# Kernel tuning notes

Hardware: AMD Instinct MI355X
Metric: run time of the kernel (lower is better)

## Reference

```python
import jax, jax.numpy as jnp
import numpy as np

DIMS = 1024; HEAD = 16; HD = DIMS // HEAD
MAX_DIST = 1024; MAX_SPAN = 1024; TEMP_SCALE = 0.01
SCALE = HD ** -0.25  # hd^-0.25 per the torch modules


def _layer_norm(x, g, b, eps=1e-5):
    m = jnp.mean(x, -1, keepdims=True)
    v = jnp.mean((x - m) ** 2, -1, keepdims=True)
    return (x - m) * jax.lax.rsqrt(v + eps) * g + b


def _forward(x, ln_a_g, ln_a_b, ln_b_g, ln_b_b, Wq, bq, Wk, Wv, bv, Wc, bc, Wp, bp, Wo, bo):
    B, S, D = x.shape
    local = _layer_norm(x, ln_a_g, ln_a_b)
    globe = _layer_norm(x, ln_b_g, ln_b_b)
    # --- global path: QueryModule/KeyModule/ValueModule + AttentionCombiner SDPA (mask=None) ---
    q = (globe @ Wq.T + bq).reshape(B, S, HEAD, HD).transpose(0, 2, 1, 3) * SCALE
    k = (globe @ Wk.T).reshape(B, S, HEAD, HD).transpose(0, 2, 1, 3) * SCALE
    v = (globe @ Wv.T + bv).reshape(B, S, HEAD, HD).transpose(0, 2, 1, 3)
    # SDPA applies its own 1/sqrt(hd) on top of the modules' hd^-0.25 scalings (faithful to torch)
    scores = jnp.einsum('bhqd,bhkd->bhqk', q, k) / jnp.sqrt(jnp.asarray(HD, x.dtype))
    w = jax.nn.softmax(scores, -1)
    g_out = jnp.einsum('bhqk,bhkd->bhqd', w, v).transpose(0, 2, 1, 3).reshape(B, S, D)
    g_out = g_out @ Wc.T + bc
    # --- span predictor; torch uses span_scale.mean().item() which detaches -> stop_gradient ---
    span_scale = jax.nn.sigmoid(jnp.mean(g_out, 1) @ Wp.T + bp)  # [B,1]
    span_mean = jax.lax.stop_gradient(jnp.mean(span_scale))
    span_len = jnp.minimum(jnp.floor(MAX_SPAN * span_mean).astype(jnp.int32), S)
    eff = jnp.maximum(jnp.minimum(span_len, MAX_DIST), 1)  # eff_span (>=1 to keep softmax finite)
    temp = 1.0 + TEMP_SCALE * (1.0 - span_mean)  # sharpen=True branch
    # --- local AdaptiveSpan path: q[:, :eff], k[:, :eff], v[:, :eff] expressed as masking
    #     so shapes stay static under jit; rows >= eff are the zero-padding of the span output.
    lh = local.reshape(B, S, HEAD, HD).transpose(0, 2, 1, 3)  # [B,H,S,hd]
    ls = jnp.einsum('bhqd,bhkd->bhqk', lh, lh) / temp * SCALE
    valid = jnp.arange(S) < eff
    ls = jnp.where(valid[None, None, None, :], ls, jnp.asarray(-1e30, x.dtype))
    lw = jax.nn.softmax(ls, -1)
    l_out = jnp.einsum('bhqk,bhkd->bhqd', lw, lh).transpose(0, 2, 1, 3).reshape(B, S, D)
    l_out = jnp.where(valid[None, :, None], l_out, jnp.asarray(0.0, x.dtype))
    combined = jnp.concatenate([l_out, g_out], -1)  # [B,S,2D]
    return combined @ Wo.T + bo


def setup_inputs() -> dict:
    key = jax.random.key(0)
    ks = jax.random.split(key, 8)
    B, S = 2, 1024
    nrm = lambda k, sh, std=0.02: jax.random.normal(k, sh, jnp.float32) * std
    return {
        'x': jax.random.normal(ks[0], (B, S, DIMS), jnp.float32),
        'ln_a_g': jnp.ones(DIMS, jnp.float32), 'ln_a_b': jnp.zeros(DIMS, jnp.float32),
        'ln_b_g': jnp.ones(DIMS, jnp.float32), 'ln_b_b': jnp.zeros(DIMS, jnp.float32),
        'Wq': nrm(ks[1], (DIMS, DIMS)), 'bq': jnp.zeros(DIMS, jnp.float32),
        'Wk': nrm(ks[2], (DIMS, DIMS)),
        'Wv': nrm(ks[3], (DIMS, DIMS)), 'bv': jnp.zeros(DIMS, jnp.float32),
        'Wc': nrm(ks[4], (DIMS, DIMS)), 'bc': jnp.zeros(DIMS, jnp.float32),
        'Wp': nrm(ks[5], (1, DIMS), (2.0 / (DIMS + 1)) ** 0.5), 'bp': jnp.zeros(1, jnp.float32),
        'Wo': nrm(ks[6], (DIMS, 2 * DIMS)), 'bo': jnp.zeros(DIMS, jnp.float32),
    }


def reference(x, ln_a_g, ln_a_b, ln_b_g, ln_b_b, Wq, bq, Wk, Wv, bv, Wc, bc, Wp, bp, Wo, bo):
    return _forward(x, ln_a_g, ln_a_b, ln_b_g, ln_b_b, Wq, bq, Wk, Wv, bv, Wc, bc, Wp, bp, Wo, bo)
```

## Files before the change

kernel.cpp:

```cpp
#include <hip/hip_runtime.h>
#include <math.h>

#define S_LEN 1024
#define DIMS  1024
#define NHEAD 16
#define HD    64
#define BATCH 2
#define MROWS (BATCH * S_LEN)
#define LOG2E 1.44269504088896f

typedef unsigned short us;
typedef __attribute__((ext_vector_type(8))) __bf16 bf8_t;
typedef __attribute__((ext_vector_type(8))) unsigned short us8_t;
typedef __attribute__((ext_vector_type(4))) unsigned short us4_t;
typedef __attribute__((ext_vector_type(4))) float f32x4;
typedef __attribute__((ext_vector_type(4))) unsigned int u32x4;

static __device__ inline us f2bf(float f) {
    unsigned int u = __builtin_bit_cast(unsigned int, f);
    unsigned int r = u + 0x7fffu + ((u >> 16) & 1u);
    return (us)(r >> 16);
}
static __device__ inline float bf2f(us v) {
    unsigned int u = ((unsigned int)v) << 16;
    return __builtin_bit_cast(float, u);
}
static __device__ inline unsigned int pk2bf(float lo, float hi) {
    unsigned int r;
    asm("v_cvt_pk_bf16_f32 %0, %1, %2" : "=v"(r) : "v"(lo), "v"(hi));
    return r;
}
static __device__ inline f32x4 mfma16(us8_t a, us8_t b, f32x4 c) {
    return __builtin_amdgcn_mfma_f32_16x16x32_bf16(
        __builtin_bit_cast(bf8_t, a), __builtin_bit_cast(bf8_t, b), c, 0, 0, 0);
}

__global__ __launch_bounds__(256) void prep_kernel(
    const float* __restrict__ s0, const float* __restrict__ s1,
    const float* __restrict__ s2, const float* __restrict__ s3,
    const float* __restrict__ s4,
    us* __restrict__ d0, us* __restrict__ d1, us* __restrict__ d2,
    us* __restrict__ d3, us* __restrict__ d4,
    const float* __restrict__ x,
    const float* __restrict__ ga, const float* __restrict__ ba,
    const float* __restrict__ gb, const float* __restrict__ bb,
    us* __restrict__ outA, us* __restrict__ outB,
    unsigned int* __restrict__ ctr)
{
    int bidx = blockIdx.x;
    int t = threadIdx.x;
    if (bidx == 0 && t == 0) *ctr = 0u;
    if (bidx < 6144) {
        const float* src; us* dst; int blk;
        if (bidx < 1024)      { src = s0; dst = d0; blk = bidx; }
        else if (bidx < 2048) { src = s1; dst = d1; blk = bidx - 1024; }
        else if (bidx < 3072) { src = s2; dst = d2; blk = bidx - 2048; }
        else if (bidx < 4096) { src = s3; dst = d3; blk = bidx - 3072; }
        else                  { src = s4; dst = d4; blk = bidx - 4096; }
        size_t idx = (size_t)blk * 1024 + t * 4;
        float4 v = *(const float4*)(src + idx);
        us4_t ot;
        ot[0] = f2bf(v.x); ot[1] = f2bf(v.y); ot[2] = f2bf(v.z); ot[3] = f2bf(v.w);
        *(us4_t*)(dst + idx) = ot;
        return;
    }
    int row = bidx - 6144;
    const float* xr = x + (size_t)row * DIMS;
    float4 v = *(const float4*)(xr + t * 4);
    float sum1 = v.x + v.y + v.z + v.w;
    float sumq = v.x * v.x + v.y * v.y + v.z * v.z + v.w * v.w;
#pragma unroll
    for (int o = 32; o > 0; o >>= 1) {
        sum1 += __shfl_down(sum1, o, 64);
        sumq += __shfl_down(sumq, o, 64);
    }
    __shared__ float rs[4], rq[4];
    int wid = t >> 6, lane = t & 63;
    if (lane == 0) { rs[wid] = sum1; rq[wid] = sumq; }
    __syncthreads();
    float T1 = rs[0] + rs[1] + rs[2] + rs[3];
    float T2 = rq[0] + rq[1] + rq[2] + rq[3];
    float mean = T1 * (1.0f / DIMS);
    float var  = T2 * (1.0f / DIMS) - mean * mean;
    float inv  = 1.0f / sqrtf(var + 1e-5f);
    float4 vga = *(const float4*)(ga + t * 4);
    float4 vba = *(const float4*)(ba + t * 4);
    float4 vgb = *(const float4*)(gb + t * 4);
    float4 vbb = *(const float4*)(bb + t * 4);
    float nx = (v.x - mean) * inv, ny = (v.y - mean) * inv;
    float nz = (v.z - mean) * inv, nw = (v.w - mean) * inv;
    us4_t oa, ob;
    oa[0] = f2bf(nx * vga.x + vba.x); oa[1] = f2bf(ny * vga.y + vba.y);
    oa[2] = f2bf(nz * vga.z + vba.z); oa[3] = f2bf(nw * vga.w + vba.w);
    ob[0] = f2bf(nx * vgb.x + vbb.x); ob[1] = f2bf(ny * vgb.y + vbb.y);
    ob[2] = f2bf(nz * vgb.z + vbb.z); ob[3] = f2bf(nw * vgb.w + vbb.w);
    *(us4_t*)(outA + (size_t)row * DIMS + t * 4) = oa;
    *(us4_t*)(outB + (size_t)row * DIMS + t * 4) = ob;
}

template <int OUTBF>
static __device__ __forceinline__ void gemm128_body(
    const us* __restrict__ A, int lda,
    const us* __restrict__ W, int ldw,
    const float* __restrict__ bias,
    void* __restrict__ Cp, int ldc, int K,
    int bm, int bn, us* As, us* Bs)
{
    int tid = threadIdx.x;
    int w = tid >> 6, l = tid & 63, l15 = l & 15, lhi = l >> 4;
    int wr = w >> 1, wc = w & 1;
    f32x4 acc[4][2];
#pragma unroll
    for (int m = 0; m < 4; ++m) { acc[m][0] = (f32x4){0,0,0,0}; acc[m][1] = (f32x4){0,0,0,0}; }
    int srow = tid >> 3;
    int scol8 = tid & 7;
    int sl = (scol8 ^ (srow & 7)) * 8;
    const us* Ap = A + (size_t)(bm + srow) * lda + scol8 * 8;
    const us* Wpt = W + (size_t)(bn + srow) * ldw + scol8 * 8;
    us8_t a0 = *(const us8_t*)(Ap);
    us8_t a1 = *(const us8_t*)(Ap + (size_t)32 * lda);
    us8_t a2 = *(const us8_t*)(Ap + (size_t)64 * lda);
    us8_t a3 = *(const us8_t*)(Ap + (size_t)96 * lda);
    us8_t b0 = *(const us8_t*)(Wpt);
    us8_t b1 = *(const us8_t*)(Wpt + (size_t)32 * ldw);
    int xorbase = l15 & 7;
    for (int kt = 0; kt < K; kt += 64) {
        __syncthreads();
        *(us8_t*)&As[(srow +  0) * 64 + sl] = a0;
        *(us8_t*)&As[(srow + 32) * 64 + sl] = a1;
        *(us8_t*)&As[(srow + 64) * 64 + sl] = a2;
        *(us8_t*)&As[(srow + 96) * 64 + sl] = a3;
        *(us8_t*)&Bs[(srow +  0) * 64 + sl] = b0;
        *(us8_t*)&Bs[(srow + 32) * 64 + sl] = b1;
        __syncthreads();
        if (kt + 64 < K) {
            a0 = *(const us8_t*)(Ap + kt + 64);
            a1 = *(const us8_t*)(Ap + (size_t)32 * lda + kt + 64);
            a2 = *(const us8_t*)(Ap + (size_t)64 * lda + kt + 64);
            a3 = *(const us8_t*)(Ap + (size_t)96 * lda + kt + 64);
            b0 = *(const us8_t*)(Wpt + kt + 64);
            b1 = *(const us8_t*)(Wpt + (size_t)32 * ldw + kt + 64);
        }
#pragma unroll
        for (int kk = 0; kk < 2; ++kk) {
            int xo = ((kk * 4 + lhi) ^ xorbase) * 8;
            us8_t af[4], bfr[2];
#pragma unroll
            for (int m = 0; m < 4; ++m)
                af[m] = *(const us8_t*)&As[(wr * 64 + m * 16 + l15) * 64 + xo];
#pragma unroll
            for (int n = 0; n < 2; ++n)
                bfr[n] = *(const us8_t*)&Bs[(wc * 32 + n * 16 + l15) * 64 + xo];
#pragma unroll
            for (int m = 0; m < 4; ++m)
#pragma unroll
                for (int n = 0; n < 2; ++n)
                    acc[m][n] = mfma16(af[m], bfr[n], acc[m][n]);
        }
    }
    float bvv[2] = {0.f, 0.f};
    if (bias) {
#pragma unroll
        for (int n = 0; n < 2; ++n)
            bvv[n] = bias[bn + wc * 32 + n * 16 + l15];
    }
#pragma unroll
    for (int m = 0; m < 4; ++m) {
#pragma unroll
        for (int n = 0; n < 2; ++n) {
            int row = bm + wr * 64 + m * 16 + lhi * 4;
            int col = bn + wc * 32 + n * 16 + l15;
            if (OUTBF) {
                us* Cb = (us*)Cp;
                unsigned int p01 = pk2bf(acc[m][n][0] + bvv[n], acc[m][n][1] + bvv[n]);
                unsigned int p23 = pk2bf(acc[m][n][2] + bvv[n], acc[m][n][3] + bvv[n]);
                Cb[(size_t)(row + 0) * ldc + col] = (us)p01;
                Cb[(size_t)(row + 1) * ldc + col] = (us)(p01 >> 16);
                Cb[(size_t)(row + 2) * ldc + col] = (us)p23;
                Cb[(size_t)(row + 3) * ldc + col] = (us)(p23 >> 16);
            } else {
                float* Cf = (float*)Cp;
#pragma unroll
                for (int r = 0; r < 4; ++r)
                    Cf[(size_t)(row + r) * ldc + col] = acc[m][n][r] + bvv[n];
            }
        }
    }
}

__global__ __launch_bounds__(256) void gemm_qkv(
    const us* __restrict__ A,
    const us* __restrict__ Wq, const us* __restrict__ Wk, const us* __restrict__ Wv,
    const float* __restrict__ bq, const float* __restrict__ bv,
    us* __restrict__ qo, us* __restrict__ ko, us* __restrict__ vo)
{
    __shared__ __align__(16) us As[128 * 64];
    __shared__ __align__(16) us Bs[64 * 64];
    int which = blockIdx.x >> 4;
    int bn = (blockIdx.x & 15) * 64, bm = blockIdx.y * 128;
    const us* W = (which == 0) ? Wq : ((which == 1) ? Wk : Wv);
    const float* bias2 = (which == 0) ? bq : ((which == 2) ? bv : nullptr);
    us* Out = (which == 0) ? qo : ((which == 1) ? ko : vo);
    gemm128_body<1>(A, DIMS, W, DIMS, bias2, Out, DIMS, DIMS, bm, bn, As, Bs);
}

template <int OUTBF>
__global__ __launch_bounds__(256) void gemm_bf16(
    const us* __restrict__ A, int lda,
    const us* __restrict__ W, int ldw,
    const float* __restrict__ bias,
    void* __restrict__ Cp, int ldc, int K)
{
    __shared__ __align__(16) us As[64 * 64];
    __shared__ __align__(16) us Bs[64 * 64];
    int tid = threadIdx.x;
    int w = tid >> 6, l = tid & 63, l15 = l & 15, lhi = l >> 4;
    int wr = w >> 1, wc = w & 1;
    int bm = blockIdx.y * 64, bn = blockIdx.x * 64;
    f32x4 acc[2][2] = {{{0,0,0,0},{0,0,0,0}},{{0,0,0,0},{0,0,0,0}}};
    int srow = tid >> 3;
    int scol8 = tid & 7;
    const us* Ap = A + (size_t)(bm + srow) * lda + scol8 * 8;
    const us* Wpt = W + (size_t)(bn + srow) * ldw + scol8 * 8;
    int sl = (scol8 ^ (srow & 7)) * 8;
    us8_t a0 = *(const us8_t*)(Ap);
    us8_t a1 = *(const us8_t*)(Ap + (size_t)32 * lda);
    us8_t b0 = *(const us8_t*)(Wpt);
    us8_t b1 = *(const us8_t*)(Wpt + (size_t)32 * ldw);
    int xorbase = l15 & 7;
    for (int kt = 0; kt < K; kt += 64) {
        __syncthreads();
        *(us8_t*)&As[srow * 64 + sl] = a0;
        *(us8_t*)&As[(srow + 32) * 64 + sl] = a1;
        *(us8_t*)&Bs[srow * 64 + sl] = b0;
        *(us8_t*)&Bs[(srow + 32) * 64 + sl] = b1;
        __syncthreads();
        if (kt + 64 < K) {
            a0 = *(const us8_t*)(Ap + kt + 64);
            a1 = *(const us8_t*)(Ap + (size_t)32 * lda + kt + 64);
            b0 = *(const us8_t*)(Wpt + kt + 64);
            b1 = *(const us8_t*)(Wpt + (size_t)32 * ldw + kt + 64);
        }
#pragma unroll
        for (int kk = 0; kk < 2; ++kk) {
            int xo = ((kk * 4 + lhi) ^ xorbase) * 8;
            us8_t af[2], bfr[2];
#pragma unroll
            for (int m = 0; m < 2; ++m)
                af[m] = *(const us8_t*)&As[(wr * 32 + m * 16 + l15) * 64 + xo];
#pragma unroll
            for (int n = 0; n < 2; ++n)
                bfr[n] = *(const us8_t*)&Bs[(wc * 32 + n * 16 + l15) * 64 + xo];
#pragma unroll
            for (int m = 0; m < 2; ++m)
#pragma unroll
                for (int n = 0; n < 2; ++n)
                    acc[m][n] = mfma16(af[m], bfr[n], acc[m][n]);
        }
    }
    float bvv[2] = {0.f, 0.f};
    if (bias) {
#pragma unroll
        for (int n = 0; n < 2; ++n)
            bvv[n] = bias[bn + wc * 32 + n * 16 + l15];
    }
#pragma unroll
    for (int m = 0; m < 2; ++m) {
#pragma unroll
        for (int n = 0; n < 2; ++n) {
            int row = bm + wr * 32 + m * 16 + lhi * 4;
            int col = bn + wc * 32 + n * 16 + l15;
            if (OUTBF) {
                us* Cb = (us*)Cp;
                unsigned int p01 = pk2bf(acc[m][n][0] + bvv[n], acc[m][n][1] + bvv[n]);
                unsigned int p23 = pk2bf(acc[m][n][2] + bvv[n], acc[m][n][3] + bvv[n]);
                Cb[(size_t)(row + 0) * ldc + col] = (us)p01;
                Cb[(size_t)(row + 1) * ldc + col] = (us)(p01 >> 16);
                Cb[(size_t)(row + 2) * ldc + col] = (us)p23;
                Cb[(size_t)(row + 3) * ldc + col] = (us)(p23 >> 16);
            } else {
                float* Cf = (float*)Cp;
#pragma unroll
                for (int r = 0; r < 4; ++r)
                    Cf[(size_t)(row + r) * ldc + col] = acc[m][n][r] + bvv[n];
            }
        }
    }
}

template <int LOCAL>
__global__ __launch_bounds__(512) void attn_mfma(
    const us* __restrict__ Q, const us* __restrict__ K,
    const us* __restrict__ V, us* __restrict__ O, int ldo,
    const float* __restrict__ span)
{
    __shared__ __align__(16) us Ks[2][64 * 64];
    __shared__ __align__(16) us Vt[2][64 * 64];
    __shared__ __align__(16) us Ps[8][1024];

    int bid = blockIdx.x;
    int xcd = bid & 7, slot = bid >> 3;
    int p = xcd + 8 * (slot >> 4);
    int q0blk = (slot & 15) * 64;
    int h = p & 15, b = p >> 4;

    int tid = threadIdx.x;
    int w = tid >> 6, l = tid & 63;
    int l15 = l & 15, lhi = l >> 4;
    int wq = w & 3, wk = w >> 2;

    float scale; int eff;
    if (LOCAL) { scale = span[1] * LOG2E; eff = (int)span[0]; }
    else       { scale = LOG2E / 64.0f; eff = S_LEN; }
    int ntiles = LOCAL ? ((eff + 63) >> 6) : 16;
    int nIter = (ntiles + 1) >> 1;

    int qrow = q0blk + wq * 16 + l15;
    const us* qptr = Q + ((size_t)(b * S_LEN + qrow)) * DIMS + h * HD + lhi * 8;
    us8_t qf[2];
    qf[0] = *(const us8_t*)(qptr);
    qf[1] = *(const us8_t*)(qptr + 32);

    f32x4 o[4] = {{0,0,0,0},{0,0,0,0},{0,0,0,0},{0,0,0,0}};
    float m_r[4] = {-1e30f, -1e30f, -1e30f, -1e30f};
    float l_r[4] = {0.f, 0.f, 0.f, 0.f};

    int half = tid >> 8;
    int t0 = tid & 255;
    int krow = t0 >> 3, kcol8 = t0 & 7;
    int ksl = (kcol8 ^ (krow & 7)) * 8;
    int vkb = t0 & 15, vdb = t0 >> 4;
    const us* Kb = K + ((size_t)(b * S_LEN)) * DIMS + h * HD;
    const us* Vb = V + ((size_t)(b * S_LEN)) * DIMS + h * HD;

    unsigned pbase = (unsigned)(unsigned long long)&Ps[w][0];
    unsigned paddr = pbase + (unsigned)(l * 8);

    us8_t kc0, kc1;
    us4_t vr0, vr1, vr2, vr3;
    if (half < ntiles) {
        const us* kp = Kb + (size_t)(half * 64 + krow) * DIMS + kcol8 * 8;
        kc0 = *(const us8_t*)kp;
        kc1 = *(const us8_t*)(kp + (size_t)32 * DIMS);
        const us* vp = Vb + (size_t)(half * 64 + vkb * 4) * DIMS + vdb * 4;
        vr0 = *(const us4_t*)(vp);
        vr1 = *(const us4_t*)(vp + DIMS);
        vr2 = *(const us4_t*)(vp + 2 * DIMS);
        vr3 = *(const us4_t*)(vp + 3 * DIMS);
    }

    for (int i = 0; i < nIter; ++i) {
        __syncthreads();
        if (2 * i + half < ntiles) {
            *(us8_t*)&Ks[half][krow * 64 + ksl] = kc0;
            *(us8_t*)&Ks[half][(krow + 32) * 64 + ksl] = kc1;
#pragma unroll
            for (int j = 0; j < 4; ++j) {
                int d = vdb * 4 + j;
                us4_t wv;
                wv[0] = vr0[j]; wv[1] = vr1[j]; wv[2] = vr2[j]; wv[3] = vr3[j];
                int slotv = (vkb >> 1) ^ (d & 7);
                *(us4_t*)&Vt[half][d * 64 + slotv * 8 + (vkb & 1) * 4] = wv;
            }
        }
        __syncthreads();
        int nt2 = 2 * (i + 1) + half;
        if (nt2 < ntiles) {
            const us* kp = Kb + (size_t)(nt2 * 64 + krow) * DIMS + kcol8 * 8;
            kc0 = *(const us8_t*)kp;
            kc1 = *(const us8_t*)(kp + (size_t)32 * DIMS);
            const us* vp = Vb + (size_t)(nt2 * 64 + vkb * 4) * DIMS + vdb * 4;
            vr0 = *(const us4_t*)(vp);
            vr1 = *(const us4_t*)(vp + DIMS);
            vr2 = *(const us4_t*)(vp + 2 * DIMS);
            vr3 = *(const us4_t*)(vp + 3 * DIMS);
        }
        int kt = 2 * i + wk;
        if (kt < ntiles) {
            f32x4 s4[4] = {{0,0,0,0},{0,0,0,0},{0,0,0,0},{0,0,0,0}};
            __builtin_amdgcn_s_setprio(1);
#pragma unroll
            for (int kk = 0; kk < 2; ++kk) {
                int xo = ((kk * 4 + lhi) ^ (l15 & 7)) * 8;
#pragma unroll
                for (int n = 0; n < 4; ++n) {
                    us8_t bk = *(const us8_t*)&Ks[wk][(n * 16 + l15) * 64 + xo];
                    s4[n] = mfma16(qf[kk], bk, s4[n]);
                }
            }
            __builtin_amdgcn_s_setprio(0);
#pragma unroll
            for (int n = 0; n < 4; ++n) {
                s4[n] *= scale;
                if (LOCAL) {
                    int key = kt * 64 + n * 16 + l15;
                    if (key >= eff) {
                        s4[n][0] = -1e30f; s4[n][1] = -1e30f;
                        s4[n][2] = -1e30f; s4[n][3] = -1e30f;
                    }
                }
            }
            float tl[4];
#pragma unroll
            for (int r = 0; r < 4; ++r)
                tl[r] = fmaxf(fmaxf(s4[0][r], s4[1][r]), fmaxf(s4[2][r], s4[3][r]));
            int ex = (tl[0] > m_r[0] + 11.5f) | (tl[1] > m_r[1] + 11.5f) |
                     (tl[2] > m_r[2] + 11.5f) | (tl[3] > m_r[3] + 11.5f);
            if (__any(ex)) {
#pragma unroll
                for (int msk = 1; msk <= 8; msk <<= 1) {
#pragma unroll
                    for (int r = 0; r < 4; ++r)
                        tl[r] = fmaxf(tl[r], __shfl_xor(tl[r], msk, 64));
                }
                float fac[4];
#pragma unroll
                for (int r = 0; r < 4; ++r) {
                    float mn = fmaxf(m_r[r], tl[r]);
                    fac[r] = exp2f(m_r[r] - mn);
                    m_r[r] = mn;
                    l_r[r] *= fac[r];
                }
#pragma unroll
                for (int n = 0; n < 4; ++n) {
                    o[n][0] *= fac[0]; o[n][1] *= fac[1];
                    o[n][2] *= fac[2]; o[n][3] *= fac[3];
                }
            }
#pragma unroll
            for (int n = 0; n < 4; ++n) {
                float p0 = exp2f(s4[n][0] - m_r[0]);
                float p1 = exp2f(s4[n][1] - m_r[1]);
                float p2 = exp2f(s4[n][2] - m_r[2]);
                float p3 = exp2f(s4[n][3] - m_r[3]);
                l_r[0] += p0; l_r[1] += p1; l_r[2] += p2; l_r[3] += p3;
                unsigned int p01 = pk2bf(p0, p1);
                unsigned int p23 = pk2bf(p2, p3);
                int idx = (n >> 1) * 512 + ((l15 & 4) ? 256 : 0)
                        + ((n & 1) * 2 + (l15 >> 3)) * 64 + (l15 & 3) * 16 + lhi * 4;
                *(uint2*)&Ps[w][idx] = make_uint2(p01, p23);
            }
            unsigned long long ta0, ta1, ta2, ta3;
            asm volatile(
                "ds_read_b64_tr_b16 %0, %4\n\t"
                "ds_read_b64_tr_b16 %1, %4 offset:512\n\t"
                "ds_read_b64_tr_b16 %2, %4 offset:1024\n\t"
                "ds_read_b64_tr_b16 %3, %4 offset:1536\n\t"
                "s_waitcnt lgkmcnt(0)"
                : "=&v"(ta0), "=&v"(ta1), "=&v"(ta2), "=&v"(ta3)
                : "v"(paddr)
                : "memory");
            __builtin_amdgcn_sched_barrier(0);
            u32x4 w0 = {(unsigned)ta0, (unsigned)(ta0 >> 32),
                        (unsigned)ta1, (unsigned)(ta1 >> 32)};
            u32x4 w1 = {(unsigned)ta2, (unsigned)(ta2 >> 32),
                        (unsigned)ta3, (unsigned)(ta3 >> 32)};
            us8_t pa0 = __builtin_bit_cast(us8_t, w0);
            us8_t pa1 = __builtin_bit_cast(us8_t, w1);
            __builtin_amdgcn_s_setprio(1);
#pragma unroll
            for (int kk = 0; kk < 2; ++kk) {
                int xo = ((kk * 4 + lhi) ^ (l15 & 7)) * 8;
                us8_t pa = kk ? pa1 : pa0;
#pragma unroll
                for (int n = 0; n < 4; ++n) {
                    us8_t vb = *(const us8_t*)&Vt[wk][(n * 16 + l15) * 64 + xo];
                    o[n] = mfma16(pa, vb, o[n]);
                }
            }
            __builtin_amdgcn_s_setprio(0);
        }
    }

#pragma unroll
    for (int msk = 1; msk <= 8; msk <<= 1) {
#pragma unroll
        for (int r = 0; r < 4; ++r)
            l_r[r] += __shfl_xor(l_r[r], msk, 64);
    }

    __syncthreads();
    float* obuf = (float*)&Ks[0][0];
    float* mlb  = (float*)&Vt[0][0];
    if (wk == 1) {
#pragma unroll
        for (int n = 0; n < 4; ++n)
#pragma unroll
            for (int r = 0; r < 4; ++r)
                obuf[wq * 1024 + (lhi * 4 + r) * 64 + n * 16 + l15] = o[n][r];
        if (l15 == 0) {
#pragma unroll
            for (int r = 0; r < 4; ++r) {
                mlb[wq * 32 + (lhi * 4 + r) * 2 + 0] = m_r[r];
                mlb[wq * 32 + (lhi * 4 + r) * 2 + 1] = l_r[r];
            }
        }
    }
    __syncthreads();
    if (wk == 0) {
        float f0[4], f1[4], rcp[4];
#pragma unroll
        for (int r = 0; r < 4; ++r) {
            int row = lhi * 4 + r;
            float m1 = mlb[wq * 32 + row * 2 + 0];
            float l1 = mlb[wq * 32 + row * 2 + 1];
            float ms = fmaxf(m_r[r], m1);
            f0[r] = exp2f(m_r[r] - ms);
            f1[r] = exp2f(m1 - ms);
            rcp[r] = 1.0f / (l_r[r] * f0[r] + l1 * f1[r]);
        }
#pragma unroll
        for (int n = 0; n < 4; ++n) {
            float vv[4];
#pragma unroll
            for (int r = 0; r < 4; ++r) {
                int row = q0blk + wq * 16 + lhi * 4 + r;
                float val = (o[n][r] * f0[r] +
                             obuf[wq * 1024 + (lhi * 4 + r) * 64 + n * 16 + l15] * f1[r]) * rcp[r];
                if (LOCAL && row >= eff) val = 0.0f;
                vv[r] = val;
            }
            int row0 = q0blk + wq * 16 + lhi * 4;
            unsigned int p01 = pk2bf(vv[0], vv[1]);
            unsigned int p23 = pk2bf(vv[2], vv[3]);
            size_t base = ((size_t)(b * S_LEN + row0)) * ldo + h * HD + n * 16 + l15;
            O[base + 0 * ldo] = (us)p01;
            O[base + 1 * ldo] = (us)(p01 >> 16);
            O[base + 2 * ldo] = (us)p23;
            O[base + 3 * ldo] = (us)(p23 >> 16);
        }
    }
}

__global__ __launch_bounds__(256) void span_fused(
    const us* __restrict__ gout, const float* __restrict__ Wp,
    const float* __restrict__ bp,
    float* __restrict__ partials, float* __restrict__ spanbuf,
    unsigned int* __restrict__ ctr)
{
    int slice = blockIdx.x;
    int b = blockIdx.y;
    int t = threadIdx.x;
    float4 wp = *(const float4*)(Wp + t * 4);
    float acc = 0;
    int srow0 = slice * 128;
    for (int s = srow0; s < srow0 + 128; ++s) {
        us4_t g = *(const us4_t*)(gout + (size_t)(b * S_LEN + s) * 2048 + t * 4);
        acc += bf2f(g[0]) * wp.x + bf2f(g[1]) * wp.y + bf2f(g[2]) * wp.z + bf2f(g[3]) * wp.w;
    }
#pragma unroll
    for (int o = 32; o > 0; o >>= 1) acc += __shfl_down(acc, o, 64);
    __shared__ float r[4];
    int wid = t >> 6, lane = t & 63;
    if (lane == 0) r[wid] = acc;
    __syncthreads();
    if (t == 0) {
        partials[b * 8 + slice] = r[0] + r[1] + r[2] + r[3];
        __threadfence();
        unsigned int old = atomicAdd(ctr, 1u);
        if (old == 15u) {
            __threadfence();
            float l0 = 0, l1 = 0;
            for (int i = 0; i < 8; ++i) { l0 += partials[i]; l1 += partials[8 + i]; }
            l0 = l0 * (1.0f / 1024.0f) + bp[0];
            l1 = l1 * (1.0f / 1024.0f) + bp[0];
            float sg0 = 1.0f / (1.0f + expf(-l0));
            float sg1 = 1.0f / (1.0f + expf(-l1));
            float sm = 0.5f * (sg0 + sg1);
            int sl = (int)floorf(1024.0f * sm);
            int eff = sl; if (eff > 1024) eff = 1024; if (eff < 1) eff = 1;
            float temp = 1.0f + 0.01f * (1.0f - sm);
            spanbuf[0] = (float)eff;
            spanbuf[1] = 0.35355339059327378f / temp;
        }
    }
}

extern "C" void kernel_launch(void* const* d_in, const int* in_sizes, int n_in,
                              void* d_out, int out_size, void* d_ws, size_t ws_size,
                              hipStream_t stream)
{
    (void)in_sizes; (void)n_in; (void)out_size; (void)ws_size;
    const float* x   = (const float*)d_in[0];
    const float* lag = (const float*)d_in[1];
    const float* lab = (const float*)d_in[2];
    const float* lbg = (const float*)d_in[3];
    const float* lbb = (const float*)d_in[4];
    const float* Wq  = (const float*)d_in[5];
    const float* bq  = (const float*)d_in[6];
    const float* Wk  = (const float*)d_in[7];
    const float* Wv  = (const float*)d_in[8];
    const float* bv  = (const float*)d_in[9];
    const float* Wc  = (const float*)d_in[10];
    const float* bc  = (const float*)d_in[11];
    const float* Wp  = (const float*)d_in[12];
    const float* bp  = (const float*)d_in[13];
    const float* Wo  = (const float*)d_in[14];
    const float* bo  = (const float*)d_in[15];
    float* out = (float*)d_out;
    us* wsu = (us*)d_ws;

    const size_t NM = (size_t)MROWS * DIMS;
    us* lnAbf = wsu;
    us* lnBbf = wsu + NM;
    us* gattbf = lnBbf;
    us* qbf   = wsu + 2 * NM;
    us* kbf   = wsu + 3 * NM;
    us* vbf   = wsu + 4 * NM;
    us* combbf = qbf;
    us* Wqbf  = wsu + 5 * NM;
    us* Wkbf  = Wqbf + DIMS * DIMS;
    us* Wvbf  = Wkbf + DIMS * DIMS;
    us* Wcbf  = Wvbf + DIMS * DIMS;
    us* Wobf  = Wcbf + DIMS * DIMS;
    float* partials = (float*)(Wobf + 2 * DIMS * DIMS);
    float* spanbuf  = partials + 16;
    unsigned int* spanctr = (unsigned int*)(spanbuf + 8);

    prep_kernel<<<8192, 256, 0, stream>>>(Wq, Wk, Wv, Wc, Wo,
                                          Wqbf, Wkbf, Wvbf, Wcbf, Wobf,
                                          x, lag, lab, lbg, lbb, lnAbf, lnBbf,
                                          spanctr);

    gemm_qkv<<<dim3(48, MROWS / 128), 256, 0, stream>>>(
        lnBbf, Wqbf, Wkbf, Wvbf, bq, bv, qbf, kbf, vbf);

    attn_mfma<0><<<512, 512, 0, stream>>>(qbf, kbf, vbf, gattbf, DIMS, nullptr);

    gemm_bf16<1><<<dim3(DIMS / 64, MROWS / 64), 256, 0, stream>>>(
        gattbf, DIMS, Wcbf, DIMS, bc, combbf + 1024, 2048, DIMS);

    span_fused<<<dim3(8, BATCH), 256, 0, stream>>>(combbf + 1024, Wp, bp,
                                                   partials, spanbuf, spanctr);

    attn_mfma<1><<<512, 512, 0, stream>>>(lnAbf, lnAbf, lnAbf, combbf, 2048, spanbuf);

    gemm_bf16<0><<<dim3(DIMS / 64, MROWS / 64), 256, 0, stream>>>(
        combbf, 2048, Wobf, 2048, bo, out, DIMS, 2 * DIMS);
}
```

Before: 126.6 us.

## Double-buffer GEMM tiles with direct global-to-LDS loads and widen span reduction

Rewrites the QKV, combiner and output GEMM main loops to issue global_load_lds copies straight into a double-buffered, XOR-swizzled shared-memory tile. The next K tile is fetched while the current one feeds the MFMAs, which removes the register staging and one barrier per iteration. Separately, the span-predictor reduction now uses 128 slices per batch instead of 8 so the column sum runs across many more blocks. In exchange the GEMMs use twice the LDS, which may reduce occupancy, and the last-block reduction serially sums 256 partials.

```diff
diff --git a/kernel.cpp b/kernel.cpp
--- a/kernel.cpp
+++ b/kernel.cpp
@@ -33,6 +33,11 @@
 static __device__ inline f32x4 mfma16(us8_t a, us8_t b, f32x4 c) {
     return __builtin_amdgcn_mfma_f32_16x16x32_bf16(
         __builtin_bit_cast(bf8_t, a), __builtin_bit_cast(bf8_t, b), c, 0, 0, 0);
+}
+static __device__ __forceinline__ void gload16(const us* g, us* l) {
+    __builtin_amdgcn_global_load_lds(
+        (__attribute__((address_space(1))) void*)(g),
+        (__attribute__((address_space(3))) void*)(l), 16, 0, 0);
 }
 
 __global__ __launch_bounds__(256) void prep_kernel(
@@ -99,7 +104,7 @@
 }
 
 template <int OUTBF>
-static __device__ __forceinline__ void gemm128_body(
+static __device__ __forceinline__ void gemm128g_body(
     const us* __restrict__ A, int lda,
     const us* __restrict__ W, int ldw,
     const float* __restrict__ bias,
@@ -112,45 +117,60 @@
     f32x4 acc[4][2];
 #pragma unroll
     for (int m = 0; m < 4; ++m) { acc[m][0] = (f32x4){0,0,0,0}; acc[m][1] = (f32x4){0,0,0,0}; }
-    int srow = tid >> 3;
-    int scol8 = tid & 7;
-    int sl = (scol8 ^ (srow & 7)) * 8;
-    const us* Ap = A + (size_t)(bm + srow) * lda + scol8 * 8;
-    const us* Wpt = W + (size_t)(bn + srow) * ldw + scol8 * 8;
-    us8_t a0 = *(const us8_t*)(Ap);
-    us8_t a1 = *(const us8_t*)(Ap + (size_t)32 * lda);
-    us8_t a2 = *(const us8_t*)(Ap + (size_t)64 * lda);
-    us8_t a3 = *(const us8_t*)(Ap + (size_t)96 * lda);
-    us8_t b0 = *(const us8_t*)(Wpt);
-    us8_t b1 = *(const us8_t*)(Wpt + (size_t)32 * ldw);
-    int xorbase = l15 & 7;
-    for (int kt = 0; kt < K; kt += 64) {
+    int lr8 = l >> 3, lc = l & 7;
+
+    int nK = K >> 6;
+    {
+#pragma unroll
+        for (int c = 0; c < 4; ++c) {
+            int R0 = c * 32 + w * 8;
+            int row = R0 + lr8;
+            int col8 = lc ^ (row & 7);
+            gload16(A + (size_t)(bm + row) * lda + col8 * 8, As + R0 * 64);
+        }
+#pragma unroll
+        for (int c = 0; c < 2; ++c) {
+            int R0 = c * 32 + w * 8;
+            int row = R0 + lr8;
+            int col8 = lc ^ (row & 7);
+            gload16(W + (size_t)(bn + row) * ldw + col8 * 8, Bs + R0 * 64);
+        }
+    }
+    for (int t = 0; t < nK; ++t) {
+        int cur = t & 1;
         __syncthreads();
-        *(us8_t*)&As[(srow +  0) * 64 + sl] = a0;
-        *(us8_t*)&As[(srow + 32) * 64 + sl] = a1;
-        *(us8_t*)&As[(srow + 64) * 64 + sl] = a2;
-        *(us8_t*)&As[(srow + 96) * 64 + sl] = a3;
-        *(us8_t*)&Bs[(srow +  0) * 64 + sl] = b0;
-        *(us8_t*)&Bs[(srow + 32) * 64 + sl] = b1;
-        __syncthreads();
-        if (kt + 64 < K) {
-            a0 = *(const us8_t*)(Ap + kt + 64);
-            a1 = *(const us8_t*)(Ap + (size_t)32 * lda + kt + 64);
-            a2 = *(const us8_t*)(Ap + (size_t)64 * lda + kt + 64);
-            a3 = *(const us8_t*)(Ap + (size_t)96 * lda + kt + 64);
-            b0 = *(const us8_t*)(Wpt + kt + 64);
-            b1 = *(const us8_t*)(Wpt + (size_t)32 * ldw + kt + 64);
-        }
+        if (t + 1 < nK) {
+            int nxt = cur ^ 1;
+            int kt = (t + 1) * 64;
+#pragma unroll
+            for (int c = 0; c < 4; ++c) {
+                int R0 = c * 32 + w * 8;
+                int row = R0 + lr8;
+                int col8 = lc ^ (row & 7);
+                gload16(A + (size_t)(bm + row) * lda + kt + col8 * 8,
+                        As + nxt * (128 * 64) + R0 * 64);
+            }
+#pragma unroll
+            for (int c = 0; c < 2; ++c) {
+                int R0 = c * 32 + w * 8;
+                int row = R0 + lr8;
+                int col8 = lc ^ (row & 7);
+                gload16(W + (size_t)(bn + row) * ldw + kt + col8 * 8,
+                        Bs + nxt * (64 * 64) + R0 * 64);
+            }
+        }
+        const us* Ab = As + cur * (128 * 64);
+        const us* Bb = Bs + cur * (64 * 64);
 #pragma unroll
         for (int kk = 0; kk < 2; ++kk) {
-            int xo = ((kk * 4 + lhi) ^ xorbase) * 8;
+            int xo = ((kk * 4 + lhi) ^ (l15 & 7)) * 8;
             us8_t af[4], bfr[2];
 #pragma unroll
             for (int m = 0; m < 4; ++m)
-                af[m] = *(const us8_t*)&As[(wr * 64 + m * 16 + l15) * 64 + xo];
+                af[m] = *(const us8_t*)&Ab[(wr * 64 + m * 16 + l15) * 64 + xo];
 #pragma unroll
             for (int n = 0; n < 2; ++n)
-                bfr[n] = *(const us8_t*)&Bs[(wc * 32 + n * 16 + l15) * 64 + xo];
+                bfr[n] = *(const us8_t*)&Bb[(wc * 32 + n * 16 + l15) * 64 + xo];
 #pragma unroll
             for (int m = 0; m < 4; ++m)
 #pragma unroll
@@ -194,63 +214,69 @@
     const float* __restrict__ bq, const float* __restrict__ bv,
     us* __restrict__ qo, us* __restrict__ ko, us* __restrict__ vo)
 {
-    __shared__ __align__(16) us As[128 * 64];
-    __shared__ __align__(16) us Bs[64 * 64];
+    __shared__ __align__(16) us As[2][128 * 64];
+    __shared__ __align__(16) us Bs[2][64 * 64];
     int which = blockIdx.x >> 4;
     int bn = (blockIdx.x & 15) * 64, bm = blockIdx.y * 128;
     const us* W = (which == 0) ? Wq : ((which == 1) ? Wk : Wv);
     const float* bias2 = (which == 0) ? bq : ((which == 2) ? bv : nullptr);
     us* Out = (which == 0) ? qo : ((which == 1) ? ko : vo);
-    gemm128_body<1>(A, DIMS, W, DIMS, bias2, Out, DIMS, DIMS, bm, bn, As, Bs);
+    gemm128g_body<1>(A, DIMS, W, DIMS, bias2, Out, DIMS, DIMS, bm, bn,
+                     &As[0][0], &Bs[0][0]);
 }
 
 template <int OUTBF>
-__global__ __launch_bounds__(256) void gemm_bf16(
+__global__ __launch_bounds__(256) void gemm64g(
     const us* __restrict__ A, int lda,
     const us* __restrict__ W, int ldw,
     const float* __restrict__ bias,
     void* __restrict__ Cp, int ldc, int K)
 {
-    __shared__ __align__(16) us As[64 * 64];
-    __shared__ __align__(16) us Bs[64 * 64];
+    __shared__ __align__(16) us As[2][64 * 64];
+    __shared__ __align__(16) us Bs[2][64 * 64];
     int tid = threadIdx.x;
     int w = tid >> 6, l = tid & 63, l15 = l & 15, lhi = l >> 4;
     int wr = w >> 1, wc = w & 1;
     int bm = blockIdx.y * 64, bn = blockIdx.x * 64;
     f32x4 acc[2][2] = {{{0,0,0,0},{0,0,0,0}},{{0,0,0,0},{0,0,0,0}}};
-    int srow = tid >> 3;
-    int scol8 = tid & 7;
-    const us* Ap = A + (size_t)(bm + srow) * lda + scol8 * 8;
-    const us* Wpt = W + (size_t)(bn + srow) * ldw + scol8 * 8;
-    int sl = (scol8 ^ (srow & 7)) * 8;
-    us8_t a0 = *(const us8_t*)(Ap);
-    us8_t a1 = *(const us8_t*)(Ap + (size_t)32 * lda);
-    us8_t b0 = *(const us8_t*)(Wpt);
-    us8_t b1 = *(const us8_t*)(Wpt + (size_t)32 * ldw);
-    int xorbase = l15 & 7;
-    for (int kt = 0; kt < K; kt += 64) {
+    int lr8 = l >> 3, lc = l & 7;
+
+    int nK = K >> 6;
+    {
+#pragma unroll
+        for (int c = 0; c < 2; ++c) {
+            int R0 = c * 32 + w * 8;
+            int row = R0 + lr8;
+            int col8 = lc ^ (row & 7);
+            gload16(A + (size_t)(bm + row) * lda + col8 * 8, &As[0][R0 * 64]);
+            gload16(W + (size_t)(bn + row) * ldw + col8 * 8, &Bs[0][R0 * 64]);
+        }
+    }
+    for (int t = 0; t < nK; ++t) {
+        int cur = t & 1;
         __syncthreads();
-        *(us8_t*)&As[srow * 64 + sl] = a0;
-        *(us8_t*)&As[(srow + 32) * 64 + sl] = a1;
-        *(us8_t*)&Bs[srow * 64 + sl] = b0;
-        *(us8_t*)&Bs[(srow + 32) * 64 + sl] = b1;
-        __syncthreads();
-        if (kt + 64 < K) {
-            a0 = *(const us8_t*)(Ap + kt + 64);
-            a1 = *(const us8_t*)(Ap + (size_t)32 * lda + kt + 64);
-            b0 = *(const us8_t*)(Wpt + kt + 64);
-            b1 = *(const us8_t*)(Wpt + (size_t)32 * ldw + kt + 64);
+        if (t + 1 < nK) {
+            int nxt = cur ^ 1;
+            int kt = (t + 1) * 64;
+#pragma unroll
+            for (int c = 0; c < 2; ++c) {
+                int R0 = c * 32 + w * 8;
+                int row = R0 + lr8;
+                int col8 = lc ^ (row & 7);
+                gload16(A + (size_t)(bm + row) * lda + kt + col8 * 8, &As[nxt][R0 * 64]);
+                gload16(W + (size_t)(bn + row) * ldw + kt + col8 * 8, &Bs[nxt][R0 * 64]);
+            }
         }
 #pragma unroll
         for (int kk = 0; kk < 2; ++kk) {
-            int xo = ((kk * 4 + lhi) ^ xorbase) * 8;
+            int xo = ((kk * 4 + lhi) ^ (l15 & 7)) * 8;
             us8_t af[2], bfr[2];
 #pragma unroll
             for (int m = 0; m < 2; ++m)
-                af[m] = *(const us8_t*)&As[(wr * 32 + m * 16 + l15) * 64 + xo];
+                af[m] = *(const us8_t*)&As[cur][(wr * 32 + m * 16 + l15) * 64 + xo];
 #pragma unroll
             for (int n = 0; n < 2; ++n)
-                bfr[n] = *(const us8_t*)&Bs[(wc * 32 + n * 16 + l15) * 64 + xo];
+                bfr[n] = *(const us8_t*)&Bs[cur][(wc * 32 + n * 16 + l15) * 64 + xo];
 #pragma unroll
             for (int m = 0; m < 2; ++m)
 #pragma unroll
@@ -543,8 +569,8 @@
     int t = threadIdx.x;
     float4 wp = *(const float4*)(Wp + t * 4);
     float acc = 0;
-    int srow0 = slice * 128;
-    for (int s = srow0; s < srow0 + 128; ++s) {
+    int srow0 = slice * 8;
+    for (int s = srow0; s < srow0 + 8; ++s) {
         us4_t g = *(const us4_t*)(gout + (size_t)(b * S_LEN + s) * 2048 + t * 4);
         acc += bf2f(g[0]) * wp.x + bf2f(g[1]) * wp.y + bf2f(g[2]) * wp.z + bf2f(g[3]) * wp.w;
     }
@@ -555,13 +581,13 @@
     if (lane == 0) r[wid] = acc;
     __syncthreads();
     if (t == 0) {
-        partials[b * 8 + slice] = r[0] + r[1] + r[2] + r[3];
+        partials[b * 128 + slice] = r[0] + r[1] + r[2] + r[3];
         __threadfence();
         unsigned int old = atomicAdd(ctr, 1u);
-        if (old == 15u) {
+        if (old == 255u) {
             __threadfence();
             float l0 = 0, l1 = 0;
-            for (int i = 0; i < 8; ++i) { l0 += partials[i]; l1 += partials[8 + i]; }
+            for (int i = 0; i < 128; ++i) { l0 += partials[i]; l1 += partials[128 + i]; }
             l0 = l0 * (1.0f / 1024.0f) + bp[0];
             l1 = l1 * (1.0f / 1024.0f) + bp[0];
             float sg0 = 1.0f / (1.0f + expf(-l0));
@@ -614,7 +640,7 @@
     us* Wcbf  = Wvbf + DIMS * DIMS;
     us* Wobf  = Wcbf + DIMS * DIMS;
     float* partials = (float*)(Wobf + 2 * DIMS * DIMS);
-    float* spanbuf  = partials + 16;
+    float* spanbuf  = partials + 256;
     unsigned int* spanctr = (unsigned int*)(spanbuf + 8);
 
     prep_kernel<<<8192, 256, 0, stream>>>(Wq, Wk, Wv, Wc, Wo,
@@ -627,14 +653,14 @@
 
     attn_mfma<0><<<512, 512, 0, stream>>>(qbf, kbf, vbf, gattbf, DIMS, nullptr);
 
-    gemm_bf16<1><<<dim3(DIMS / 64, MROWS / 64), 256, 0, stream>>>(
+    gemm64g<1><<<dim3(DIMS / 64, MROWS / 64), 256, 0, stream>>>(
         gattbf, DIMS, Wcbf, DIMS, bc, combbf + 1024, 2048, DIMS);
 
-    span_fused<<<dim3(8, BATCH), 256, 0, stream>>>(combbf + 1024, Wp, bp,
-                                                   partials, spanbuf, spanctr);
+    span_fused<<<dim3(128, BATCH), 256, 0, stream>>>(combbf + 1024, Wp, bp,
+                                                     partials, spanbuf, spanctr);
 
     attn_mfma<1><<<512, 512, 0, stream>>>(lnAbf, lnAbf, lnAbf, combbf, 2048, spanbuf);
 
-    gemm_bf16<0><<<dim3(DIMS / 64, MROWS / 64), 256, 0, stream>>>(
+    gemm64g<0><<<dim3(DIMS / 64, MROWS / 64), 256, 0, stream>>>(
         combbf, 2048, Wobf, 2048, bo, out, DIMS, 2 * DIMS);
 }
```

Measured after the change: 128.3 us. No clear change (+1.3%).

## Fuse fp32 weight-to-bf16 conversion into GEMM tile loads and split span reduction wider

Applied to the files above, without the earlier changes.

Drops the separate weight conversion pass in the prep kernel. The GEMMs now load fp32 weights directly and convert them to bf16 while staging into shared memory. This removes writing and re-reading about 12 MB of bf16 weights, but each GEMM block now reads twice the weight bytes and converts redundantly across the M tiles. The span reduction also uses 32 slices per batch instead of 8, for more parallelism.

```diff
diff --git a/kernel.cpp b/kernel.cpp
--- a/kernel.cpp
+++ b/kernel.cpp
@@ -30,41 +30,29 @@
     asm("v_cvt_pk_bf16_f32 %0, %1, %2" : "=v"(r) : "v"(lo), "v"(hi));
     return r;
 }
+static __device__ inline us8_t cvt8(float4 a, float4 b) {
+    unsigned p0 = pk2bf(a.x, a.y), p1 = pk2bf(a.z, a.w);
+    unsigned p2 = pk2bf(b.x, b.y), p3 = pk2bf(b.z, b.w);
+    us8_t r;
+    r[0] = (us)p0; r[1] = (us)(p0 >> 16); r[2] = (us)p1; r[3] = (us)(p1 >> 16);
+    r[4] = (us)p2; r[5] = (us)(p2 >> 16); r[6] = (us)p3; r[7] = (us)(p3 >> 16);
+    return r;
+}
 static __device__ inline f32x4 mfma16(us8_t a, us8_t b, f32x4 c) {
     return __builtin_amdgcn_mfma_f32_16x16x32_bf16(
         __builtin_bit_cast(bf8_t, a), __builtin_bit_cast(bf8_t, b), c, 0, 0, 0);
 }
 
-__global__ __launch_bounds__(256) void prep_kernel(
-    const float* __restrict__ s0, const float* __restrict__ s1,
-    const float* __restrict__ s2, const float* __restrict__ s3,
-    const float* __restrict__ s4,
-    us* __restrict__ d0, us* __restrict__ d1, us* __restrict__ d2,
-    us* __restrict__ d3, us* __restrict__ d4,
+__global__ __launch_bounds__(256) void ln_kernel(
     const float* __restrict__ x,
     const float* __restrict__ ga, const float* __restrict__ ba,
     const float* __restrict__ gb, const float* __restrict__ bb,
     us* __restrict__ outA, us* __restrict__ outB,
     unsigned int* __restrict__ ctr)
 {
-    int bidx = blockIdx.x;
+    int row = blockIdx.x;
     int t = threadIdx.x;
-    if (bidx == 0 && t == 0) *ctr = 0u;
-    if (bidx < 6144) {
-        const float* src; us* dst; int blk;
-        if (bidx < 1024)      { src = s0; dst = d0; blk = bidx; }
-        else if (bidx < 2048) { src = s1; dst = d1; blk = bidx - 1024; }
-        else if (bidx < 3072) { src = s2; dst = d2; blk = bidx - 2048; }
-        else if (bidx < 4096) { src = s3; dst = d3; blk = bidx - 3072; }
-        else                  { src = s4; dst = d4; blk = bidx - 4096; }
-        size_t idx = (size_t)blk * 1024 + t * 4;
-        float4 v = *(const float4*)(src + idx);
-        us4_t ot;
-        ot[0] = f2bf(v.x); ot[1] = f2bf(v.y); ot[2] = f2bf(v.z); ot[3] = f2bf(v.w);
-        *(us4_t*)(dst + idx) = ot;
-        return;
-    }
-    int row = bidx - 6144;
+    if (row == 0 && t == 0) *ctr = 0u;
     const float* xr = x + (size_t)row * DIMS;
     float4 v = *(const float4*)(xr + t * 4);
     float sum1 = v.x + v.y + v.z + v.w;
@@ -98,12 +86,11 @@
     *(us4_t*)(outB + (size_t)row * DIMS + t * 4) = ob;
 }
 
-template <int OUTBF>
 static __device__ __forceinline__ void gemm128_body(
     const us* __restrict__ A, int lda,
-    const us* __restrict__ W, int ldw,
+    const float* __restrict__ Wf, int ldw,
     const float* __restrict__ bias,
-    void* __restrict__ Cp, int ldc, int K,
+    us* __restrict__ Cp, int ldc, int K,
     int bm, int bn, us* As, us* Bs)
 {
     int tid = threadIdx.x;
@@ -116,34 +103,38 @@
     int scol8 = tid & 7;
     int sl = (scol8 ^ (srow & 7)) * 8;
     const us* Ap = A + (size_t)(bm + srow) * lda + scol8 * 8;
-    const us* Wpt = W + (size_t)(bn + srow) * ldw + scol8 * 8;
+    const float* Wp0 = Wf + (size_t)(bn + srow) * ldw + scol8 * 8;
+    const float* Wp1 = Wf + (size_t)(bn + srow + 32) * ldw + scol8 * 8;
     us8_t a0 = *(const us8_t*)(Ap);
     us8_t a1 = *(const us8_t*)(Ap + (size_t)32 * lda);
     us8_t a2 = *(const us8_t*)(Ap + (size_t)64 * lda);
     us8_t a3 = *(const us8_t*)(Ap + (size_t)96 * lda);
-    us8_t b0 = *(const us8_t*)(Wpt);
-    us8_t b1 = *(const us8_t*)(Wpt + (size_t)32 * ldw);
-    int xorbase = l15 & 7;
+    float4 w0a = *(const float4*)(Wp0);
+    float4 w0b = *(const float4*)(Wp0 + 4);
+    float4 w1a = *(const float4*)(Wp1);
+    float4 w1b = *(const float4*)(Wp1 + 4);
     for (int kt = 0; kt < K; kt += 64) {
         __syncthreads();
         *(us8_t*)&As[(srow +  0) * 64 + sl] = a0;
         *(us8_t*)&As[(srow + 32) * 64 + sl] = a1;
         *(us8_t*)&As[(srow + 64) * 64 + sl] = a2;
         *(us8_t*)&As[(srow + 96) * 64 + sl] = a3;
-        *(us8_t*)&Bs[(srow +  0) * 64 + sl] = b0;
-        *(us8_t*)&Bs[(srow + 32) * 64 + sl] = b1;
+        *(us8_t*)&Bs[(srow +  0) * 64 + sl] = cvt8(w0a, w0b);
+        *(us8_t*)&Bs[(srow + 32) * 64 + sl] = cvt8(w1a, w1b);
         __syncthreads();
         if (kt + 64 < K) {
             a0 = *(const us8_t*)(Ap + kt + 64);
             a1 = *(const us8_t*)(Ap + (size_t)32 * lda + kt + 64);
             a2 = *(const us8_t*)(Ap + (size_t)64 * lda + kt + 64);
             a3 = *(const us8_t*)(Ap + (size_t)96 * lda + kt + 64);
-            b0 = *(const us8_t*)(Wpt + kt + 64);
-            b1 = *(const us8_t*)(Wpt + (size_t)32 * ldw + kt + 64);
+            w0a = *(const float4*)(Wp0 + kt + 64);
+            w0b = *(const float4*)(Wp0 + kt + 68);
+            w1a = *(const float4*)(Wp1 + kt + 64);
+            w1b = *(const float4*)(Wp1 + kt + 68);
         }
 #pragma unroll
         for (int kk = 0; kk < 2; ++kk) {
-            int xo = ((kk * 4 + lhi) ^ xorbase) * 8;
+            int xo = ((kk * 4 + lhi) ^ (l15 & 7)) * 8;
             us8_t af[4], bfr[2];
 #pragma unroll
             for (int m = 0; m < 4; ++m)
@@ -170,27 +161,19 @@
         for (int n = 0; n < 2; ++n) {
             int row = bm + wr * 64 + m * 16 + lhi * 4;
             int col = bn + wc * 32 + n * 16 + l15;
-            if (OUTBF) {
-                us* Cb = (us*)Cp;
-                unsigned int p01 = pk2bf(acc[m][n][0] + bvv[n], acc[m][n][1] + bvv[n]);
-                unsigned int p23 = pk2bf(acc[m][n][2] + bvv[n], acc[m][n][3] + bvv[n]);
-                Cb[(size_t)(row + 0) * ldc + col] = (us)p01;
-                Cb[(size_t)(row + 1) * ldc + col] = (us)(p01 >> 16);
-                Cb[(size_t)(row + 2) * ldc + col] = (us)p23;
-                Cb[(size_t)(row + 3) * ldc + col] = (us)(p23 >> 16);
-            } else {
-                float* Cf = (float*)Cp;
-#pragma unroll
-                for (int r = 0; r < 4; ++r)
-                    Cf[(size_t)(row + r) * ldc + col] = acc[m][n][r] + bvv[n];
-            }
+            unsigned int p01 = pk2bf(acc[m][n][0] + bvv[n], acc[m][n][1] + bvv[n]);
+            unsigned int p23 = pk2bf(acc[m][n][2] + bvv[n], acc[m][n][3] + bvv[n]);
+            Cp[(size_t)(row + 0) * ldc + col] = (us)p01;
+            Cp[(size_t)(row + 1) * ldc + col] = (us)(p01 >> 16);
+            Cp[(size_t)(row + 2) * ldc + col] = (us)p23;
+            Cp[(size_t)(row + 3) * ldc + col] = (us)(p23 >> 16);
         }
     }
 }
 
 __global__ __launch_bounds__(256) void gemm_qkv(
     const us* __restrict__ A,
-    const us* __restrict__ Wq, const us* __restrict__ Wk, const us* __restrict__ Wv,
+    const float* __restrict__ Wq, const float* __restrict__ Wk, const float* __restrict__ Wv,
     const float* __restrict__ bq, const float* __restrict__ bv,
     us* __restrict__ qo, us* __restrict__ ko, us* __restrict__ vo)
 {
@@ -198,52 +181,54 @@
     __shared__ __align__(16) us Bs[64 * 64];
     int which = blockIdx.x >> 4;
     int bn = (blockIdx.x & 15) * 64, bm = blockIdx.y * 128;
-    const us* W = (which == 0) ? Wq : ((which == 1) ? Wk : Wv);
+    const float* W = (which == 0) ? Wq : ((which == 1) ? Wk : Wv);
     const float* bias2 = (which == 0) ? bq : ((which == 2) ? bv : nullptr);
     us* Out = (which == 0) ? qo : ((which == 1) ? ko : vo);
-    gemm128_body<1>(A, DIMS, W, DIMS, bias2, Out, DIMS, DIMS, bm, bn, As, Bs);
+    gemm128_body(A, DIMS, W, DIMS, bias2, Out, DIMS, DIMS, bm, bn, As, Bs);
 }
 
 template <int OUTBF>
-__global__ __launch_bounds__(256) void gemm_bf16(
+static __device__ __forceinline__ void gemm64_body(
     const us* __restrict__ A, int lda,
-    const us* __restrict__ W, int ldw,
+    const float* __restrict__ Wf, int ldw,
     const float* __restrict__ bias,
-    void* __restrict__ Cp, int ldc, int K)
-{
-    __shared__ __align__(16) us As[64 * 64];
-    __shared__ __align__(16) us Bs[64 * 64];
+    void* __restrict__ Cp, int ldc, int K,
+    int bm, int bn, us* As, us* Bs)
+{
     int tid = threadIdx.x;
     int w = tid >> 6, l = tid & 63, l15 = l & 15, lhi = l >> 4;
     int wr = w >> 1, wc = w & 1;
-    int bm = blockIdx.y * 64, bn = blockIdx.x * 64;
     f32x4 acc[2][2] = {{{0,0,0,0},{0,0,0,0}},{{0,0,0,0},{0,0,0,0}}};
     int srow = tid >> 3;
     int scol8 = tid & 7;
     const us* Ap = A + (size_t)(bm + srow) * lda + scol8 * 8;
-    const us* Wpt = W + (size_t)(bn + srow) * ldw + scol8 * 8;
+    const float* Wp0 = Wf + (size_t)(bn + srow) * ldw + scol8 * 8;
+    const float* Wp1 = Wf + (size_t)(bn + srow + 32) * ldw + scol8 * 8;
     int sl = (scol8 ^ (srow & 7)) * 8;
     us8_t a0 = *(const us8_t*)(Ap);
     us8_t a1 = *(const us8_t*)(Ap + (size_t)32 * lda);
-    us8_t b0 = *(const us8_t*)(Wpt);
-    us8_t b1 = *(const us8_t*)(Wpt + (size_t)32 * ldw);
-    int xorbase = l15 & 7;
+    float4 w0a = *(const float4*)(Wp0);
+    float4 w0b = *(const float4*)(Wp0 + 4);
+    float4 w1a = *(const float4*)(Wp1);
+    float4 w1b = *(const float4*)(Wp1 + 4);
     for (int kt = 0; kt < K; kt += 64) {
         __syncthreads();
         *(us8_t*)&As[srow * 64 + sl] = a0;
         *(us8_t*)&As[(srow + 32) * 64 + sl] = a1;
-        *(us8_t*)&Bs[srow * 64 + sl] = b0;
-        *(us8_t*)&Bs[(srow + 32) * 64 + sl] = b1;
+        *(us8_t*)&Bs[srow * 64 + sl] = cvt8(w0a, w0b);
+        *(us8_t*)&Bs[(srow + 32) * 64 + sl] = cvt8(w1a, w1b);
         __syncthreads();
         if (kt + 64 < K) {
             a0 = *(const us8_t*)(Ap + kt + 64);
             a1 = *(const us8_t*)(Ap + (size_t)32 * lda + kt + 64);
-            b0 = *(const us8_t*)(Wpt + kt + 64);
-            b1 = *(const us8_t*)(Wpt + (size_t)32 * ldw + kt + 64);
+            w0a = *(const float4*)(Wp0 + kt + 64);
+            w0b = *(const float4*)(Wp0 + kt + 68);
+            w1a = *(const float4*)(Wp1 + kt + 64);
+            w1b = *(const float4*)(Wp1 + kt + 68);
         }
 #pragma unroll
         for (int kk = 0; kk < 2; ++kk) {
-            int xo = ((kk * 4 + lhi) ^ xorbase) * 8;
+            int xo = ((kk * 4 + lhi) ^ (l15 & 7)) * 8;
             us8_t af[2], bfr[2];
 #pragma unroll
             for (int m = 0; m < 2; ++m)
@@ -258,12 +243,10 @@
                     acc[m][n] = mfma16(af[m], bfr[n], acc[m][n]);
         }
     }
-    float bvv[2] = {0.f, 0.f};
-    if (bias) {
-#pragma unroll
-        for (int n = 0; n < 2; ++n)
-            bvv[n] = bias[bn + wc * 32 + n * 16 + l15];
-    }
+    float bvv[2];
+#pragma unroll
+    for (int n = 0; n < 2; ++n)
+        bvv[n] = bias[bn + wc * 32 + n * 16 + l15];
 #pragma unroll
     for (int m = 0; m < 2; ++m) {
 #pragma unroll
@@ -286,6 +269,30 @@
             }
         }
     }
+}
+
+__global__ __launch_bounds__(256) void gemm_bf16out(
+    const us* __restrict__ A, int lda,
+    const float* __restrict__ W, int ldw,
+    const float* __restrict__ bias,
+    us* __restrict__ Cp, int ldc, int K)
+{
+    __shared__ __align__(16) us As[64 * 64];
+    __shared__ __align__(16) us Bs[64 * 64];
+    gemm64_body<1>(A, lda, W, ldw, bias, Cp, ldc, K,
+                   blockIdx.y * 64, blockIdx.x * 64, As, Bs);
+}
+
+__global__ __launch_bounds__(256) void gemm_f32out(
+    const us* __restrict__ A, int lda,
+    const float* __restrict__ W, int ldw,
+    const float* __restrict__ bias,
+    float* __restrict__ Cp, int ldc, int K)
+{
+    __shared__ __align__(16) us As[64 * 64];
+    __shared__ __align__(16) us Bs[64 * 64];
+    gemm64_body<0>(A, lda, W, ldw, bias, Cp, ldc, K,
+                   blockIdx.y * 64, blockIdx.x * 64, As, Bs);
 }
 
 template <int LOCAL>
@@ -543,8 +550,8 @@
     int t = threadIdx.x;
     float4 wp = *(const float4*)(Wp + t * 4);
     float acc = 0;
-    int srow0 = slice * 128;
-    for (int s = srow0; s < srow0 + 128; ++s) {
+    int srow0 = slice * 32;
+    for (int s = srow0; s < srow0 + 32; ++s) {
         us4_t g = *(const us4_t*)(gout + (size_t)(b * S_LEN + s) * 2048 + t * 4);
         acc += bf2f(g[0]) * wp.x + bf2f(g[1]) * wp.y + bf2f(g[2]) * wp.z + bf2f(g[3]) * wp.w;
     }
@@ -555,13 +562,13 @@
     if (lane == 0) r[wid] = acc;
     __syncthreads();
     if (t == 0) {
-        partials[b * 8 + slice] = r[0] + r[1] + r[2] + r[3];
+        partials[b * 32 + slice] = r[0] + r[1] + r[2] + r[3];
         __threadfence();
         unsigned int old = atomicAdd(ctr, 1u);
-        if (old == 15u) {
+        if (old == 63u) {
             __threadfence();
             float l0 = 0, l1 = 0;
-            for (int i = 0; i < 8; ++i) { l0 += partials[i]; l1 += partials[8 + i]; }
+            for (int i = 0; i < 32; ++i) { l0 += partials[i]; l1 += partials[32 + i]; }
             l0 = l0 * (1.0f / 1024.0f) + bp[0];
             l1 = l1 * (1.0f / 1024.0f) + bp[0];
             float sg0 = 1.0f / (1.0f + expf(-l0));
@@ -608,33 +615,26 @@
     us* kbf   = wsu + 3 * NM;
     us* vbf   = wsu + 4 * NM;
     us* combbf = qbf;
-    us* Wqbf  = wsu + 5 * NM;
-    us* Wkbf  = Wqbf + DIMS * DIMS;
-    us* Wvbf  = Wkbf + DIMS * DIMS;
-    us* Wcbf  = Wvbf + DIMS * DIMS;
-    us* Wobf  = Wcbf + DIMS * DIMS;
-    float* partials = (float*)(Wobf + 2 * DIMS * DIMS);
-    float* spanbuf  = partials + 16;
+    float* partials = (float*)(wsu + 5 * NM);
+    float* spanbuf  = partials + 64;
     unsigned int* spanctr = (unsigned int*)(spanbuf + 8);
 
-    prep_kernel<<<8192, 256, 0, stream>>>(Wq, Wk, Wv, Wc, Wo,
-                                          Wqbf, Wkbf, Wvbf, Wcbf, Wobf,
-                                          x, lag, lab, lbg, lbb, lnAbf, lnBbf,
-                                          spanctr);
+    ln_kernel<<<MROWS, 256, 0, stream>>>(x, lag, lab, lbg, lbb,
+                                         lnAbf, lnBbf, spanctr);
 
     gemm_qkv<<<dim3(48, MROWS / 128), 256, 0, stream>>>(
-        lnBbf, Wqbf, Wkbf, Wvbf, bq, bv, qbf, kbf, vbf);
+        lnBbf, Wq, Wk, Wv, bq, bv, qbf, kbf, vbf);
 
     attn_mfma<0><<<512, 512, 0, stream>>>(qbf, kbf, vbf, gattbf, DIMS, nullptr);
 
-    gemm_bf16<1><<<dim3(DIMS / 64, MROWS / 64), 256, 0, stream>>>(
-        gattbf, DIMS, Wcbf, DIMS, bc, combbf + 1024, 2048, DIMS);
-
-    span_fused<<<dim3(8, BATCH), 256, 0, stream>>>(combbf + 1024, Wp, bp,
-                                                   partials, spanbuf, spanctr);
+    gemm_bf16out<<<dim3(DIMS / 64, MROWS / 64), 256, 0, stream>>>(
+        gattbf, DIMS, Wc, DIMS, bc, combbf + 1024, 2048, DIMS);
+
+    span_fused<<<dim3(32, BATCH), 256, 0, stream>>>(combbf + 1024, Wp, bp,
+                                                    partials, spanbuf, spanctr);
 
     attn_mfma<1><<<512, 512, 0, stream>>>(lnAbf, lnAbf, lnAbf, combbf, 2048, spanbuf);
 
-    gemm_bf16<0><<<dim3(DIMS / 64, MROWS / 64), 256, 0, stream>>>(
-        combbf, 2048, Wobf, 2048, bo, out, DIMS, 2 * DIMS);
-}
+    gemm_f32out<<<dim3(DIMS / 64, MROWS / 64), 256, 0, stream>>>(
+        combbf, 2048, Wo, 2048, bo, out, DIMS, 2 * DIMS);
+}
```

After: 124.2 us. Within noise of the previous version (-1.9%).
